# Optimization experiments

Measured on AMD Instinct MI355X. Metric: run time of the kernel, lower is better.

## Reference

```python
import jax, jax.numpy as jnp
import numpy as np

D_MODEL = 1024
NUM_HEADS = 16
D_HEAD = D_MODEL // NUM_HEADS


def setup_inputs() -> dict:
    key = jax.random.key(0)
    ks = jax.random.split(key, 9)
    s = 1.0 / np.sqrt(D_MODEL)
    return {
        "x": jax.random.normal(ks[0], (2, 2048, D_MODEL), dtype=jnp.float32),
        "Wq": jax.random.normal(ks[1], (D_MODEL, D_MODEL), dtype=jnp.float32) * s,
        "bq": jnp.zeros((D_MODEL,), dtype=jnp.float32),
        "Wk": jax.random.normal(ks[2], (D_MODEL, D_MODEL), dtype=jnp.float32) * s,
        "bk": jnp.zeros((D_MODEL,), dtype=jnp.float32),
        "Wv": jax.random.normal(ks[3], (D_MODEL, D_MODEL), dtype=jnp.float32) * s,
        "bv": jnp.zeros((D_MODEL,), dtype=jnp.float32),
        "Wo": jax.random.normal(ks[4], (D_MODEL, D_MODEL), dtype=jnp.float32) * s,
        "bo": jnp.zeros((D_MODEL,), dtype=jnp.float32),
    }


def reference(x, Wq, bq, Wk, bk, Wv, bv, Wo, bo):
    B, S, D = x.shape
    H, Dh = NUM_HEADS, D_HEAD

    def split_heads(t):  # [B,S,D] -> [B,H,S,Dh]
        return t.reshape(B, S, H, Dh).transpose(0, 2, 1, 3)

    # Linear layers: y = x @ W^T + b (torch nn.Linear convention)
    Q = split_heads(x @ Wq.T + bq)
    K = split_heads(x @ Wk.T + bk)
    V = split_heads(x @ Wv.T + bv)

    scale = 1.0 / jnp.sqrt(jnp.asarray(Dh, dtype=x.dtype))
    scores = jnp.einsum("bhqd,bhkd->bhqk", Q, K) * scale  # [B,H,S,S]
    attn = jax.nn.softmax(scores, axis=-1)
    context = jnp.einsum("bhqk,bhkd->bhqd", attn, V)  # [B,H,S,Dh]
    context = context.transpose(0, 2, 1, 3).reshape(B, S, D)
    return context @ Wo.T + bo
```

## Files before the change

### kernel.cpp

```cpp
#include <hip/hip_runtime.h>


#define T_TOK 4096
#define DM    1024
#define SQ    2048
#define NH    16
#define DH    64

typedef unsigned short u16;
typedef unsigned int   u32;
typedef __bf16 bf16x8 __attribute__((ext_vector_type(8)));
typedef float  f32x4  __attribute__((ext_vector_type(4)));
typedef float  f32x16 __attribute__((ext_vector_type(16)));
typedef u32    u32x4  __attribute__((ext_vector_type(4)));

__device__ __forceinline__ u16 f2bf(float f) {
  u32 u = __builtin_bit_cast(u32, f);
  u32 r = (u + 0x7FFFu + ((u >> 16) & 1u)) >> 16;
  return (u16)r;
}

#if __has_builtin(__builtin_amdgcn_cvt_pk_bf16_f32)
typedef __bf16 bf16x2 __attribute__((ext_vector_type(2)));
__device__ __forceinline__ u32 pk2bf(float a, float b) {
  bf16x2 h = __builtin_amdgcn_cvt_pk_bf16_f32(a, b);
  return __builtin_bit_cast(u32, h);
}
#else
__device__ __forceinline__ u32 pk2bf(float a, float b) {
  u32 r;
  asm("v_cvt_pk_bf16_f32 %0, %1, %2" : "=v"(r) : "v"(a), "v"(b));
  return r;
}
#endif

__device__ __forceinline__ void gld16(const void* g, void* l) {
  __builtin_amdgcn_global_load_lds(
      (const __attribute__((address_space(1))) u32*)g,
      (__attribute__((address_space(3))) u32*)l, 16, 0, 0);
}

__global__ void cast_bf16_kernel(const float* __restrict__ x,
    const float* __restrict__ w0, const float* __restrict__ w1,
    const float* __restrict__ w2, const float* __restrict__ w3,
    u16* __restrict__ xb, u16* __restrict__ o0, u16* __restrict__ o1,
    u16* __restrict__ o2, u16* __restrict__ o3)
{
  const float* src; u16* dst; int n;
  switch (blockIdx.y) {
    case 0:  src = x;  dst = xb; n = T_TOK * DM; break;
    case 1:  src = w0; dst = o0; n = DM * DM; break;
    case 2:  src = w1; dst = o1; n = DM * DM; break;
    case 3:  src = w2; dst = o2; n = DM * DM; break;
    default: src = w3; dst = o3; n = DM * DM; break;
  }
  const int stride = gridDim.x * blockDim.x;
  for (int i = blockIdx.x * blockDim.x + threadIdx.x; i * 4 < n; i += stride) {
    float4 v = ((const float4*)src)[i];
    ushort4 o;
    o.x = f2bf(v.x); o.y = f2bf(v.y); o.z = f2bf(v.z); o.w = f2bf(v.w);
    ((ushort4*)dst)[i] = o;
  }
}

__device__ __forceinline__ void gemm_core_128x128(
    u16* lds, const u16* __restrict__ Ab, const u16* __restrict__ Bb,
    f32x4 acc[4][4])
{
  u16* As = lds;
  u16* Bs = lds + 8192;
  const int tid = threadIdx.x, lane = tid & 63, w = tid >> 6;
  const int waveM = w >> 1, waveN = w & 1;
  const int col = lane & 15, quad = lane >> 4;
  const int srow = lane >> 3;
  const int sg0  = (lane & 7) ^ srow;

  for (int k0 = 0; k0 < DM; k0 += 64) {
    #pragma unroll
    for (int i = 0; i < 4; ++i) {
      const int rb = w * 32 + i * 8;
      const int sg = sg0 ^ ((rb >> 3) & 3);
      gld16(Ab + (size_t)(rb + srow) * DM + k0 + sg * 8, &As[rb * 64]);
      gld16(Bb + (size_t)(rb + srow) * DM + k0 + sg * 8, &Bs[rb * 64]);
    }
    __syncthreads();
    #pragma unroll
    for (int c = 0; c < 2; ++c) {
      bf16x8 af[4], bg[4];
      #pragma unroll
      for (int i = 0; i < 4; ++i) {
        const int row = waveM * 64 + i * 16 + col;
        const int gp = (c * 4 + quad) ^ (row & 7) ^ ((row >> 3) & 3);
        af[i] = *(const bf16x8*)&As[row * 64 + gp * 8];
      }
      #pragma unroll
      for (int j = 0; j < 4; ++j) {
        const int row = waveN * 64 + j * 16 + col;
        const int gp = (c * 4 + quad) ^ (row & 7) ^ ((row >> 3) & 3);
        bg[j] = *(const bf16x8*)&Bs[row * 64 + gp * 8];
      }
      #pragma unroll
      for (int i = 0; i < 4; ++i) {
        #pragma unroll
        for (int j = 0; j < 4; ++j)
          acc[i][j] = __builtin_amdgcn_mfma_f32_16x16x32_bf16(af[i], bg[j], acc[i][j], 0, 0, 0);
      }
    }
    __syncthreads();
  }
}

__device__ __forceinline__ void gemm_core_qk(
    u16* lds, const u16* __restrict__ Aq, const u16* __restrict__ Ak,
    const u16* __restrict__ Bb, f32x4 accQ[4][4], f32x4 accK[4][4])
{
  u16* As = lds;
  u16* A2 = lds + 8192;
  u16* Bs = lds + 16384;
  const int tid = threadIdx.x, lane = tid & 63, w = tid >> 6;
  const int waveM = w >> 1, waveN = w & 1;
  const int col = lane & 15, quad = lane >> 4;
  const int srow = lane >> 3;
  const int sg0  = (lane & 7) ^ srow;

  for (int k0 = 0; k0 < DM; k0 += 64) {
    #pragma unroll
    for (int i = 0; i < 4; ++i) {
      const int rb = w * 32 + i * 8;
      const int sg = sg0 ^ ((rb >> 3) & 3);
      const size_t off = (size_t)(rb + srow) * DM + k0 + sg * 8;
      gld16(Aq + off, &As[rb * 64]);
      gld16(Ak + off, &A2[rb * 64]);
      gld16(Bb + off, &Bs[rb * 64]);
    }
    __syncthreads();
    #pragma unroll
    for (int c = 0; c < 2; ++c) {
      bf16x8 af[4], ag[4], bg[4];
      #pragma unroll
      for (int i = 0; i < 4; ++i) {
        const int row = waveM * 64 + i * 16 + col;
        const int gp = (c * 4 + quad) ^ (row & 7) ^ ((row >> 3) & 3);
        af[i] = *(const bf16x8*)&As[row * 64 + gp * 8];
        ag[i] = *(const bf16x8*)&A2[row * 64 + gp * 8];
      }
      #pragma unroll
      for (int j = 0; j < 4; ++j) {
        const int row = waveN * 64 + j * 16 + col;
        const int gp = (c * 4 + quad) ^ (row & 7) ^ ((row >> 3) & 3);
        bg[j] = *(const bf16x8*)&Bs[row * 64 + gp * 8];
      }
      #pragma unroll
      for (int i = 0; i < 4; ++i) {
        #pragma unroll
        for (int j = 0; j < 4; ++j) {
          accQ[i][j] = __builtin_amdgcn_mfma_f32_16x16x32_bf16(af[i], bg[j], accQ[i][j], 0, 0, 0);
          accK[i][j] = __builtin_amdgcn_mfma_f32_16x16x32_bf16(ag[i], bg[j], accK[i][j], 0, 0, 0);
        }
      }
    }
    __syncthreads();
  }
}

__global__ __launch_bounds__(256, 2) void gemm_qkv_kernel(
    const u16* __restrict__ xb,
    const u16* __restrict__ Wqb, const u16* __restrict__ Wkb, const u16* __restrict__ Wvb,
    const float* __restrict__ bq, const float* __restrict__ bk, const float* __restrict__ bv,
    u16* __restrict__ Qs, u16* __restrict__ Kh, u16* __restrict__ Vt)
{
  __shared__ __align__(16) u16 smem[3 * 8192];
  const int z = blockIdx.z;
  const int tb = blockIdx.x;
  const int cb = blockIdx.y;

  const int tid = threadIdx.x;
  const int lane = tid & 63, w = tid >> 6;
  const int waveM = w >> 1, waveN = w & 1;
  const int col = lane & 15, quad = lane >> 4;
  const f32x4 zf = {0.f, 0.f, 0.f, 0.f};

  if (z == 1) {
    u16* tr = smem;
    f32x4 acc[4][4];
    #pragma unroll
    for (int i = 0; i < 4; ++i)
      #pragma unroll
      for (int j = 0; j < 4; ++j) acc[i][j] = zf;
    gemm_core_128x128(smem, xb + (size_t)(tb * 128) * DM,
                      Wvb + (size_t)(cb * 128) * DM, acc);
    #pragma unroll
    for (int j = 0; j < 4; ++j) {
      const int cl = waveN * 64 + j * 16 + col;
      const float bb = bv[cb * 128 + cl];
      #pragma unroll
      for (int i = 0; i < 4; ++i) {
        const int tl = waveM * 64 + i * 16 + quad * 4;
        ushort4 pk;
        pk.x = f2bf(acc[i][j][0] + bb); pk.y = f2bf(acc[i][j][1] + bb);
        pk.z = f2bf(acc[i][j][2] + bb); pk.w = f2bf(acc[i][j][3] + bb);
        *(ushort4*)&tr[cl * 136 + tl] = pk;
      }
    }
    __syncthreads();
    const int t0 = tb * 128;
    const int b = t0 >> 11, sBase = t0 & 2047;
    #pragma unroll
    for (int rep = 0; rep < 8; ++rep) {
      const int chunk = rep * 256 + tid;
      const int row = chunk >> 4, off = (chunk & 15) * 8;
      const int c = cb * 128 + row;
      const int h = c >> 6, d = c & 63;
      uint4 v = *(const uint4*)&tr[row * 136 + off];
      *(uint4*)&Vt[((size_t)(b * NH + h) * DH + d) * SQ + sBase + off] = v;
    }
  } else {
    f32x4 accQ[4][4], accK[4][4];
    #pragma unroll
    for (int i = 0; i < 4; ++i)
      #pragma unroll
      for (int j = 0; j < 4; ++j) { accQ[i][j] = zf; accK[i][j] = zf; }
    gemm_core_qk(smem, Wqb + (size_t)(cb * 128) * DM,
                 Wkb + (size_t)(cb * 128) * DM,
                 xb + (size_t)(tb * 128) * DM, accQ, accK);
    const float qscale = 0.18033688011112042f;
    const int chBase  = cb * 128 + waveM * 64;
    const int tokBase = tb * 128 + waveN * 64;
    #pragma unroll
    for (int i = 0; i < 4; ++i) {
      const int c0 = chBase + i * 16 + quad * 4;
      const int hh = c0 >> 6, d0 = c0 & 63;
      const float4 bbq = *(const float4*)&bq[c0];
      const float4 bbk = *(const float4*)&bk[c0];
      #pragma unroll
      for (int j = 0; j < 4; ++j) {
        const int t = tokBase + j * 16 + col;
        const int b = t >> 11, s = t & 2047;
        const size_t base = ((size_t)(b * NH + hh) * SQ + s) * DH + d0;
        ushort4 pq;
        pq.x = f2bf((accQ[i][j][0] + bbq.x) * qscale);
        pq.y = f2bf((accQ[i][j][1] + bbq.y) * qscale);
        pq.z = f2bf((accQ[i][j][2] + bbq.z) * qscale);
        pq.w = f2bf((accQ[i][j][3] + bbq.w) * qscale);
        *(ushort4*)&Qs[base] = pq;
        ushort4 pk;
        pk.x = f2bf(accK[i][j][0] + bbk.x);
        pk.y = f2bf(accK[i][j][1] + bbk.y);
        pk.z = f2bf(accK[i][j][2] + bbk.z);
        pk.w = f2bf(accK[i][j][3] + bbk.w);
        *(ushort4*)&Kh[base] = pk;
      }
    }
  }
}

__global__ __launch_bounds__(256, 4) void attn_kernel(
    const u16* __restrict__ Qs, const u16* __restrict__ Kh,
    const u16* __restrict__ Vt, u16* __restrict__ ctx)
{
  __shared__ __align__(16) char smem[33 * 1024];
  u16* KtB = (u16*)smem;
  u16* VlB = (u16*)(smem + 16384);
  f32x4* red  = (f32x4*)smem;
  float* lred = (float*)(smem + 32768);

  const int tid = threadIdx.x, lane = tid & 63, w = tid >> 6;
  const int l31 = lane & 31, h = lane >> 5;
  const int qt = w & 1, st = w >> 1;
  const int bh = blockIdx.x, q0 = blockIdx.y * 64;
  const u16* Qb = Qs + ((size_t)bh * SQ + q0) * DH;
  const u16* Kb = Kh + (size_t)bh * SQ * DH;
  const u16* Vb = Vt + (size_t)bh * DH * SQ;
  const int srow = lane >> 3;
  const int sgl  = (lane & 7) ^ srow;

  bf16x8 qreg[4];
  #pragma unroll
  for (int ks = 0; ks < 4; ++ks)
    qreg[ks] = *(const bf16x8*)(Qb + (size_t)(qt * 32 + l31) * DH + ks * 16 + h * 8);

  #pragma unroll
  for (int i = 0; i < 2; ++i) {
    const int rb = w * 16 + i * 8;
    const int sg = sgl ^ ((rb >> 3) & 3);
    gld16(Kb + (size_t)(rb + srow) * DH + sg * 8, &KtB[rb * 64]);
    gld16(Vb + (size_t)(rb + srow) * SQ + sg * 8, &VlB[rb * 64]);
  }

  f32x16 cacc[2];
  #pragma unroll
  for (int dt = 0; dt < 2; ++dt)
    #pragma unroll
    for (int e = 0; e < 16; ++e) cacc[dt][e] = 0.f;
  float l_s = 0.f;
  __syncthreads();

  for (int kt = 0; kt < SQ / 64; ++kt) {
    const int cur = kt & 1;
    u16* Kt = KtB + cur * 4096;
    u16* Vl = VlB + cur * 4096;
    if (kt + 1 < SQ / 64) {
      const int nxt = cur ^ 1, s1 = (kt + 1) * 64;
      u16* Ktn = KtB + nxt * 4096;
      u16* Vln = VlB + nxt * 4096;
      #pragma unroll
      for (int i = 0; i < 2; ++i) {
        const int rb = w * 16 + i * 8;
        const int sg = sgl ^ ((rb >> 3) & 3);
        gld16(Kb + (size_t)(s1 + rb + srow) * DH + sg * 8, &Ktn[rb * 64]);
        gld16(Vb + (size_t)(rb + srow) * SQ + s1 + sg * 8, &Vln[rb * 64]);
      }
    }

    f32x16 sacc;
    #pragma unroll
    for (int e = 0; e < 16; ++e) sacc[e] = 0.f;
    __builtin_amdgcn_s_setprio(1);
    #pragma unroll
    for (int ks = 0; ks < 4; ++ks) {
      const int row = st * 32 + l31;
      const int gp = (2 * ks + h) ^ (l31 & 7) ^ ((l31 >> 3) & 3);
      bf16x8 kf = *(const bf16x8*)&Kt[row * 64 + gp * 8];
      sacc = __builtin_amdgcn_mfma_f32_32x32x16_bf16(kf, qreg[ks], sacc, 0, 0, 0);
    }
    __builtin_amdgcn_s_setprio(0);

    u32 Pp[4][2];
    {
      float p[16];
      #pragma unroll
      for (int e = 0; e < 16; ++e)
        p[e] = __builtin_amdgcn_exp2f(sacc[e]);
      float t0 = (p[0] + p[1]) + (p[2] + p[3]);
      float t1 = (p[4] + p[5]) + (p[6] + p[7]);
      float t2 = (p[8] + p[9]) + (p[10] + p[11]);
      float t3 = (p[12] + p[13]) + (p[14] + p[15]);
      l_s += (t0 + t1) + (t2 + t3);
      #pragma unroll
      for (int rg = 0; rg < 4; ++rg) {
        Pp[rg][0] = pk2bf(p[4 * rg + 0], p[4 * rg + 1]);
        Pp[rg][1] = pk2bf(p[4 * rg + 2], p[4 * rg + 3]);
      }
    }

    __builtin_amdgcn_s_setprio(1);
    #pragma unroll
    for (int ks = 0; ks < 2; ++ks) {
      u32 own0 = h ? Pp[2 * ks + 1][0] : Pp[2 * ks][0];
      u32 own1 = h ? Pp[2 * ks + 1][1] : Pp[2 * ks][1];
      u32 snd0 = h ? Pp[2 * ks][0] : Pp[2 * ks + 1][0];
      u32 snd1 = h ? Pp[2 * ks][1] : Pp[2 * ks + 1][1];
      u32 rcv0 = (u32)__shfl_xor((int)snd0, 32, 64);
      u32 rcv1 = (u32)__shfl_xor((int)snd1, 32, 64);
      u32x4 fw;
      fw.x = h ? rcv0 : own0;
      fw.y = h ? rcv1 : own1;
      fw.z = h ? own0 : rcv0;
      fw.w = h ? own1 : rcv1;
      bf16x8 pf = __builtin_bit_cast(bf16x8, fw);
      #pragma unroll
      for (int dt = 0; dt < 2; ++dt) {
        const int row = dt * 32 + l31;
        const int gp = (4 * st + 2 * ks + h) ^ (l31 & 7) ^ ((l31 >> 3) & 3);
        bf16x8 vf = *(const bf16x8*)&Vl[row * 64 + gp * 8];
        cacc[dt] = __builtin_amdgcn_mfma_f32_32x32x16_bf16(vf, pf, cacc[dt], 0, 0, 0);
      }
    }
    __builtin_amdgcn_s_setprio(0);
    __syncthreads();
  }

  float lq = l_s + __shfl_xor(l_s, 32, 64);
  if (h == 0) lred[w * 32 + l31] = lq;
  #pragma unroll
  for (int dt = 0; dt < 2; ++dt) {
    #pragma unroll
    for (int c = 0; c < 4; ++c) {
      f32x4 ch;
      ch[0] = cacc[dt][4 * c + 0]; ch[1] = cacc[dt][4 * c + 1];
      ch[2] = cacc[dt][4 * c + 2]; ch[3] = cacc[dt][4 * c + 3];
      red[((w * 2 + dt) * 4 + c) * 64 + lane] = ch;
    }
  }
  __syncthreads();
  const int qt2 = w & 1, dt2 = w >> 1;
  const int b = bh >> 4, hd = bh & 15;
  const float lsum = lred[qt2 * 32 + l31] + lred[(2 + qt2) * 32 + l31];
  const float inv = 1.0f / lsum;
  const int s = q0 + qt2 * 32 + l31;
  #pragma unroll
  for (int c = 0; c < 4; ++c) {
    f32x4 sum = red[((qt2 * 2 + dt2) * 4 + c) * 64 + lane];
    sum += red[(((2 + qt2) * 2 + dt2) * 4 + c) * 64 + lane];
    const int d0 = dt2 * 32 + c * 8 + 4 * h;
    ushort4 pk;
    pk.x = f2bf(sum[0] * inv); pk.y = f2bf(sum[1] * inv);
    pk.z = f2bf(sum[2] * inv); pk.w = f2bf(sum[3] * inv);
    *(ushort4*)&ctx[(size_t)(b * SQ + s) * DM + hd * DH + d0] = pk;
  }
}

__device__ __forceinline__ void gemm_core_128x64(
    u16* lds, const u16* __restrict__ Ab, const u16* __restrict__ Bb,
    f32x4 acc[4][2])
{
  u16* As = lds;
  u16* Bs = lds + 8192;
  const int tid = threadIdx.x, lane = tid & 63, w = tid >> 6;
  const int waveM = w >> 1, waveN = w & 1;
  const int col = lane & 15, quad = lane >> 4;
  const int srow = lane >> 3;
  const int sg0  = (lane & 7) ^ srow;

  for (int k0 = 0; k0 < DM; k0 += 64) {
    #pragma unroll
    for (int i = 0; i < 4; ++i) {
      const int rb = w * 32 + i * 8;
      const int sg = sg0 ^ ((rb >> 3) & 3);
      gld16(Ab + (size_t)(rb + srow) * DM + k0 + sg * 8, &As[rb * 64]);
    }
    #pragma unroll
    for (int i = 0; i < 2; ++i) {
      const int rb = w * 16 + i * 8;
      const int sg = sg0 ^ ((rb >> 3) & 3);
      gld16(Bb + (size_t)(rb + srow) * DM + k0 + sg * 8, &Bs[rb * 64]);
    }
    __syncthreads();
    #pragma unroll
    for (int c = 0; c < 2; ++c) {
      bf16x8 af[4], bg[2];
      #pragma unroll
      for (int i = 0; i < 4; ++i) {
        const int row = waveM * 64 + i * 16 + col;
        const int gp = (c * 4 + quad) ^ (row & 7) ^ ((row >> 3) & 3);
        af[i] = *(const bf16x8*)&As[row * 64 + gp * 8];
      }
      #pragma unroll
      for (int j = 0; j < 2; ++j) {
        const int row = waveN * 32 + j * 16 + col;
        const int gp = (c * 4 + quad) ^ (row & 7) ^ ((row >> 3) & 3);
        bg[j] = *(const bf16x8*)&Bs[row * 64 + gp * 8];
      }
      #pragma unroll
      for (int i = 0; i < 4; ++i) {
        #pragma unroll
        for (int j = 0; j < 2; ++j)
          acc[i][j] = __builtin_amdgcn_mfma_f32_16x16x32_bf16(af[i], bg[j], acc[i][j], 0, 0, 0);
      }
    }
    __syncthreads();
  }
}

__global__ __launch_bounds__(256) void gemm_out_kernel(
    const u16* __restrict__ ctx, const u16* __restrict__ Wob,
    const float* __restrict__ bo, float* __restrict__ out)
{
  __shared__ __align__(16) u16 smem[128 * 64 + 64 * 64];
  const int tb = blockIdx.x;
  const int cb = blockIdx.y;
  const int tid = threadIdx.x, lane = tid & 63, w = tid >> 6;
  const int waveM = w >> 1, waveN = w & 1;
  const int col = lane & 15, quad = lane >> 4;

  f32x4 acc[4][2];
  const f32x4 zf = {0.f, 0.f, 0.f, 0.f};
  #pragma unroll
  for (int i = 0; i < 4; ++i) {
    #pragma unroll
    for (int j = 0; j < 2; ++j) acc[i][j] = zf;
  }

  gemm_core_128x64(smem, ctx + (size_t)(tb * 128) * DM,
                   Wob + (size_t)(cb * 64) * DM, acc);

  const int rowBase = tb * 128 + waveM * 64;
  const int colBase = cb * 64 + waveN * 32;
  #pragma unroll
  for (int j = 0; j < 2; ++j) {
    const int c = colBase + j * 16 + col;
    const float bb = bo[c];
    #pragma unroll
    for (int i = 0; i < 4; ++i) {
      #pragma unroll
      for (int r = 0; r < 4; ++r) {
        const int t = rowBase + i * 16 + quad * 4 + r;
        out[(size_t)t * DM + c] = acc[i][j][r] + bb;
      }
    }
  }
}

extern "C" void kernel_launch(void* const* d_in, const int* in_sizes, int n_in,
                              void* d_out, int out_size, void* d_ws, size_t ws_size,
                              hipStream_t stream) {
  const float* x  = (const float*)d_in[0];
  const float* Wq = (const float*)d_in[1];
  const float* bq = (const float*)d_in[2];
  const float* Wk = (const float*)d_in[3];
  const float* bk = (const float*)d_in[4];
  const float* Wv = (const float*)d_in[5];
  const float* bv = (const float*)d_in[6];
  const float* Wo = (const float*)d_in[7];
  const float* bo = (const float*)d_in[8];

  char* ws = (char*)d_ws;
  u16* xb  = (u16*)(ws);
  u16* Wqb = (u16*)(ws + (8ull  << 20));
  u16* Wkb = (u16*)(ws + (10ull << 20));
  u16* Wvb = (u16*)(ws + (12ull << 20));
  u16* Wob = (u16*)(ws + (14ull << 20));
  u16* Qs  = (u16*)(ws + (16ull << 20));
  u16* Kh  = (u16*)(ws + (24ull << 20));
  u16* Vt  = (u16*)(ws + (32ull << 20));
  u16* ctx = xb;

  cast_bf16_kernel<<<dim3(256, 5), 256, 0, stream>>>(x, Wq, Wk, Wv, Wo,
                                                     xb, Wqb, Wkb, Wvb, Wob);
  gemm_qkv_kernel<<<dim3(32, 8, 2), 256, 0, stream>>>(xb, Wqb, Wkb, Wvb,
                                                      bq, bk, bv, Qs, Kh, Vt);
  attn_kernel<<<dim3(32, 32), 256, 0, stream>>>(Qs, Kh, Vt, ctx);
  gemm_out_kernel<<<dim3(32, 16), 256, 0, stream>>>(ctx, Wob, bo, (float*)d_out);
  (void)in_sizes; (void)n_in; (void)out_size; (void)ws_size;
}
```

Measured before the change: 188.8 us.

## Give each attention wave its own 32 queries over full key tile, drop LDS reduction

The attention kernel now processes 128 queries per block, with each wave owning 32 query rows and computing scores against all 64 keys of the tile. Previously two waves split the keys and reduced partial context through shared memory. This removes the final LDS reduction and its barrier, halves the grid, and doubles K/V tile reuse per load. It also swaps the shfl_xor-based P fragment exchange for v_permlane32_swap. The cost is more registers per thread (launch bounds lowered to 2) and fewer blocks, which lowers occupancy.

```diff
diff --git a/kernel.cpp b/kernel.cpp
--- a/kernel.cpp
+++ b/kernel.cpp
@@ -254,20 +254,17 @@
   }
 }
 
-__global__ __launch_bounds__(256, 4) void attn_kernel(
+__global__ __launch_bounds__(256, 2) void attn_kernel(
     const u16* __restrict__ Qs, const u16* __restrict__ Kh,
     const u16* __restrict__ Vt, u16* __restrict__ ctx)
 {
-  __shared__ __align__(16) char smem[33 * 1024];
+  __shared__ __align__(16) char smem[32 * 1024];
   u16* KtB = (u16*)smem;
   u16* VlB = (u16*)(smem + 16384);
-  f32x4* red  = (f32x4*)smem;
-  float* lred = (float*)(smem + 32768);
 
   const int tid = threadIdx.x, lane = tid & 63, w = tid >> 6;
   const int l31 = lane & 31, h = lane >> 5;
-  const int qt = w & 1, st = w >> 1;
-  const int bh = blockIdx.x, q0 = blockIdx.y * 64;
+  const int bh = blockIdx.x, q0 = blockIdx.y * 128;
   const u16* Qb = Qs + ((size_t)bh * SQ + q0) * DH;
   const u16* Kb = Kh + (size_t)bh * SQ * DH;
   const u16* Vb = Vt + (size_t)bh * DH * SQ;
@@ -277,7 +274,7 @@
   bf16x8 qreg[4];
   #pragma unroll
   for (int ks = 0; ks < 4; ++ks)
-    qreg[ks] = *(const bf16x8*)(Qb + (size_t)(qt * 32 + l31) * DH + ks * 16 + h * 8);
+    qreg[ks] = *(const bf16x8*)(Qb + (size_t)(w * 32 + l31) * DH + ks * 16 + h * 8);
 
   #pragma unroll
   for (int i = 0; i < 2; ++i) {
@@ -312,91 +309,81 @@
       }
     }
 
-    f32x16 sacc;
-    #pragma unroll
-    for (int e = 0; e < 16; ++e) sacc[e] = 0.f;
+    f32x16 sacc0 = {}, sacc1 = {};
     __builtin_amdgcn_s_setprio(1);
     #pragma unroll
     for (int ks = 0; ks < 4; ++ks) {
-      const int row = st * 32 + l31;
-      const int gp = (2 * ks + h) ^ (l31 & 7) ^ ((l31 >> 3) & 3);
-      bf16x8 kf = *(const bf16x8*)&Kt[row * 64 + gp * 8];
-      sacc = __builtin_amdgcn_mfma_f32_32x32x16_bf16(kf, qreg[ks], sacc, 0, 0, 0);
+      const int gp = ((2 * ks + h) ^ (l31 & 7) ^ ((l31 >> 3) & 3)) * 8;
+      bf16x8 kf0 = *(const bf16x8*)&Kt[l31 * 64 + gp];
+      bf16x8 kf1 = *(const bf16x8*)&Kt[(32 + l31) * 64 + gp];
+      sacc0 = __builtin_amdgcn_mfma_f32_32x32x16_bf16(kf0, qreg[ks], sacc0, 0, 0, 0);
+      sacc1 = __builtin_amdgcn_mfma_f32_32x32x16_bf16(kf1, qreg[ks], sacc1, 0, 0, 0);
     }
     __builtin_amdgcn_s_setprio(0);
 
-    u32 Pp[4][2];
+    u32 Pp[2][4][2];
     {
-      float p[16];
-      #pragma unroll
-      for (int e = 0; e < 16; ++e)
-        p[e] = __builtin_amdgcn_exp2f(sacc[e]);
+      float p[16], q[16];
+      #pragma unroll
+      for (int e = 0; e < 16; ++e) {
+        p[e] = __builtin_amdgcn_exp2f(sacc0[e]);
+        q[e] = __builtin_amdgcn_exp2f(sacc1[e]);
+      }
       float t0 = (p[0] + p[1]) + (p[2] + p[3]);
       float t1 = (p[4] + p[5]) + (p[6] + p[7]);
       float t2 = (p[8] + p[9]) + (p[10] + p[11]);
       float t3 = (p[12] + p[13]) + (p[14] + p[15]);
-      l_s += (t0 + t1) + (t2 + t3);
+      float u0 = (q[0] + q[1]) + (q[2] + q[3]);
+      float u1 = (q[4] + q[5]) + (q[6] + q[7]);
+      float u2 = (q[8] + q[9]) + (q[10] + q[11]);
+      float u3 = (q[12] + q[13]) + (q[14] + q[15]);
+      l_s += ((t0 + t1) + (t2 + t3)) + ((u0 + u1) + (u2 + u3));
       #pragma unroll
       for (int rg = 0; rg < 4; ++rg) {
-        Pp[rg][0] = pk2bf(p[4 * rg + 0], p[4 * rg + 1]);
-        Pp[rg][1] = pk2bf(p[4 * rg + 2], p[4 * rg + 3]);
+        Pp[0][rg][0] = pk2bf(p[4 * rg + 0], p[4 * rg + 1]);
+        Pp[0][rg][1] = pk2bf(p[4 * rg + 2], p[4 * rg + 3]);
+        Pp[1][rg][0] = pk2bf(q[4 * rg + 0], q[4 * rg + 1]);
+        Pp[1][rg][1] = pk2bf(q[4 * rg + 2], q[4 * rg + 3]);
       }
     }
 
     __builtin_amdgcn_s_setprio(1);
     #pragma unroll
-    for (int ks = 0; ks < 2; ++ks) {
-      u32 own0 = h ? Pp[2 * ks + 1][0] : Pp[2 * ks][0];
-      u32 own1 = h ? Pp[2 * ks + 1][1] : Pp[2 * ks][1];
-      u32 snd0 = h ? Pp[2 * ks][0] : Pp[2 * ks + 1][0];
-      u32 snd1 = h ? Pp[2 * ks][1] : Pp[2 * ks + 1][1];
-      u32 rcv0 = (u32)__shfl_xor((int)snd0, 32, 64);
-      u32 rcv1 = (u32)__shfl_xor((int)snd1, 32, 64);
+    for (int ksg = 0; ksg < 4; ++ksg) {
+      const int hs = ksg >> 1, p2 = ksg & 1;
+      u32 a0 = Pp[hs][2 * p2][0], b0 = Pp[hs][2 * p2 + 1][0];
+      u32 a1 = Pp[hs][2 * p2][1], b1 = Pp[hs][2 * p2 + 1][1];
+      asm("v_permlane32_swap_b32 %0, %1" : "+v"(a0), "+v"(b0));
+      asm("v_permlane32_swap_b32 %0, %1" : "+v"(a1), "+v"(b1));
       u32x4 fw;
-      fw.x = h ? rcv0 : own0;
-      fw.y = h ? rcv1 : own1;
-      fw.z = h ? own0 : rcv0;
-      fw.w = h ? own1 : rcv1;
+      fw.x = a0; fw.y = a1; fw.z = b0; fw.w = b1;
       bf16x8 pf = __builtin_bit_cast(bf16x8, fw);
-      #pragma unroll
-      for (int dt = 0; dt < 2; ++dt) {
-        const int row = dt * 32 + l31;
-        const int gp = (4 * st + 2 * ks + h) ^ (l31 & 7) ^ ((l31 >> 3) & 3);
-        bf16x8 vf = *(const bf16x8*)&Vl[row * 64 + gp * 8];
-        cacc[dt] = __builtin_amdgcn_mfma_f32_32x32x16_bf16(vf, pf, cacc[dt], 0, 0, 0);
-      }
+      const int gp = ((2 * ksg + h) ^ (l31 & 7) ^ ((l31 >> 3) & 3)) * 8;
+      bf16x8 vf0 = *(const bf16x8*)&Vl[l31 * 64 + gp];
+      bf16x8 vf1 = *(const bf16x8*)&Vl[(32 + l31) * 64 + gp];
+      cacc[0] = __builtin_amdgcn_mfma_f32_32x32x16_bf16(vf0, pf, cacc[0], 0, 0, 0);
+      cacc[1] = __builtin_amdgcn_mfma_f32_32x32x16_bf16(vf1, pf, cacc[1], 0, 0, 0);
     }
     __builtin_amdgcn_s_setprio(0);
     __syncthreads();
   }
 
-  float lq = l_s + __shfl_xor(l_s, 32, 64);
-  if (h == 0) lred[w * 32 + l31] = lq;
+  const float lq = l_s + __shfl_xor(l_s, 32, 64);
+  const float inv = 1.0f / lq;
+  const int b = bh >> 4, hd = bh & 15;
+  const int s = q0 + w * 32 + l31;
   #pragma unroll
   for (int dt = 0; dt < 2; ++dt) {
     #pragma unroll
     for (int c = 0; c < 4; ++c) {
-      f32x4 ch;
-      ch[0] = cacc[dt][4 * c + 0]; ch[1] = cacc[dt][4 * c + 1];
-      ch[2] = cacc[dt][4 * c + 2]; ch[3] = cacc[dt][4 * c + 3];
-      red[((w * 2 + dt) * 4 + c) * 64 + lane] = ch;
-    }
-  }
-  __syncthreads();
-  const int qt2 = w & 1, dt2 = w >> 1;
-  const int b = bh >> 4, hd = bh & 15;
-  const float lsum = lred[qt2 * 32 + l31] + lred[(2 + qt2) * 32 + l31];
-  const float inv = 1.0f / lsum;
-  const int s = q0 + qt2 * 32 + l31;
-  #pragma unroll
-  for (int c = 0; c < 4; ++c) {
-    f32x4 sum = red[((qt2 * 2 + dt2) * 4 + c) * 64 + lane];
-    sum += red[(((2 + qt2) * 2 + dt2) * 4 + c) * 64 + lane];
-    const int d0 = dt2 * 32 + c * 8 + 4 * h;
-    ushort4 pk;
-    pk.x = f2bf(sum[0] * inv); pk.y = f2bf(sum[1] * inv);
-    pk.z = f2bf(sum[2] * inv); pk.w = f2bf(sum[3] * inv);
-    *(ushort4*)&ctx[(size_t)(b * SQ + s) * DM + hd * DH + d0] = pk;
+      const int d0 = dt * 32 + c * 8 + 4 * h;
+      ushort4 pk;
+      pk.x = f2bf(cacc[dt][4 * c + 0] * inv);
+      pk.y = f2bf(cacc[dt][4 * c + 1] * inv);
+      pk.z = f2bf(cacc[dt][4 * c + 2] * inv);
+      pk.w = f2bf(cacc[dt][4 * c + 3] * inv);
+      *(ushort4*)&ctx[(size_t)(b * SQ + s) * DM + hd * DH + d0] = pk;
+    }
   }
 }
 
@@ -519,7 +506,7 @@
                                                      xb, Wqb, Wkb, Wvb, Wob);
   gemm_qkv_kernel<<<dim3(32, 8, 2), 256, 0, stream>>>(xb, Wqb, Wkb, Wvb,
                                                       bq, bk, bv, Qs, Kh, Vt);
-  attn_kernel<<<dim3(32, 32), 256, 0, stream>>>(Qs, Kh, Vt, ctx);
+  attn_kernel<<<dim3(32, 16), 256, 0, stream>>>(Qs, Kh, Vt, ctx);
   gemm_out_kernel<<<dim3(32, 16), 256, 0, stream>>>(ctx, Wob, bo, (float*)d_out);
   (void)in_sizes; (void)n_in; (void)out_size; (void)ws_size;
 }
```

Result: faster. 180.7 us (median of 2 runs) (-4.3%).
